# Optimization experiments

Hardware: AMD Instinct MI355X
Metric: run time of the kernel (lower is better)

Reference implementation:

```python
import jax, jax.numpy as jnp
import numpy as np

# DCNv2 config (matches init_kwargs)
STRIDE, PAD, DIL = 1, 1, 1
KH, KW = 3, 3
K = KH * KW


def setup_inputs() -> dict:
    key = jax.random.key(0)
    k1, k2, k3, k4 = jax.random.split(key, 4)
    B, C, H, W = 2, 256, 96, 96
    O = 256
    inp = jax.random.normal(k1, (B, C, H, W), jnp.float32)
    # offset channels interleaved (dy, dx) per kernel tap -> 2*K channels
    offset = jax.random.normal(k2, (B, 2 * K, H, W), jnp.float32)
    # modulation mask in [0,1) (sigmoid is applied outside this module in DCN heads)
    mask = jax.random.uniform(k3, (B, K, H, W), jnp.float32)
    n = C * KH * KW
    stdv = 1.0 / float(np.sqrt(n))
    weight = jax.random.uniform(k4, (O, C, KH, KW), jnp.float32, -stdv, stdv)
    bias = jnp.zeros((O,), jnp.float32)
    return {"input": inp, "offset": offset, "mask": mask, "weight": weight, "bias": bias}


def reference(input, offset, mask, weight, bias):
    B, C, H, W = input.shape
    O = weight.shape[0]
    Ho = (H + 2 * PAD - DIL * (KH - 1) - 1) // STRIDE + 1
    Wo = (W + 2 * PAD - DIL * (KW - 1) - 1) // STRIDE + 1

    # learned per-pixel offsets: channel layout [dy_k0, dx_k0, dy_k1, dx_k1, ...]
    dy = offset[:, 0::2]  # [B,K,Ho,Wo]
    dx = offset[:, 1::2]  # [B,K,Ho,Wo]

    ky = (jnp.arange(K) // KW * DIL).astype(jnp.float32)  # kernel tap row offsets
    kx = (jnp.arange(K) % KW * DIL).astype(jnp.float32)   # kernel tap col offsets
    base_y = (jnp.arange(Ho) * STRIDE - PAD).astype(jnp.float32)
    base_x = (jnp.arange(Wo) * STRIDE - PAD).astype(jnp.float32)

    # sampling positions, [B,K,Ho,Wo]
    y = base_y[None, None, :, None] + ky[None, :, None, None] + dy
    x = base_x[None, None, None, :] + kx[None, :, None, None] + dx

    y0 = jnp.floor(y)
    x0 = jnp.floor(x)
    wy = y - y0  # bilinear fractional weights
    wx = x - x0

    inp_flat = input.reshape(B, C, H * W)

    def gather(yi, xi):
        # zero-padded bilinear corner gather: out-of-bounds -> 0
        ii = yi.astype(jnp.int32)
        jj = xi.astype(jnp.int32)
        valid = ((ii >= 0) & (ii < H) & (jj >= 0) & (jj < W)).astype(input.dtype)
        idx = jnp.clip(ii, 0, H - 1) * W + jnp.clip(jj, 0, W - 1)  # [B,K,Ho,Wo]
        v = jnp.take_along_axis(inp_flat, idx.reshape(B, 1, -1), axis=2)  # [B,C,K*Ho*Wo]
        return v * valid.reshape(B, 1, -1)

    v00 = gather(y0, x0)
    v01 = gather(y0, x0 + 1)
    v10 = gather(y0 + 1, x0)
    v11 = gather(y0 + 1, x0 + 1)

    wyf = wy.reshape(B, 1, -1)
    wxf = wx.reshape(B, 1, -1)
    sampled = (v00 * (1 - wyf) * (1 - wxf) + v01 * (1 - wyf) * wxf
               + v10 * wyf * (1 - wxf) + v11 * wyf * wxf)  # [B,C,K*Ho*Wo]

    mod = sampled * mask.reshape(B, 1, -1)           # modulation per tap/pixel
    mod = mod.reshape(B, C, K, Ho * Wo)
    out = jnp.einsum('bcks,ock->bos', mod, weight.reshape(O, C, K)) + bias[None, :, None]
    return out.reshape(B, O, Ho, Wo)
```

## Files before the change

### kernel.cpp

```cpp
#include <hip/hip_runtime.h>
#include <hip/hip_bf16.h>


#define Hh 96
#define Ww 96
#define Cc 256
#define Oo 256
#define Bb 2
#define Kk 9
#define Ss (Hh * Ww)
#define CKTOT (Cc * Kk)

typedef __bf16 bf16x8 __attribute__((ext_vector_type(8)));
typedef __bf16 bf16x2v __attribute__((ext_vector_type(2)));
typedef float f32x16 __attribute__((ext_vector_type(16)));
typedef float f32x2 __attribute__((ext_vector_type(2)));

__device__ __forceinline__ f32x2 up2(unsigned u) {
  f32x2 r;
  r.x = __uint_as_float(u << 16);
  r.y = __uint_as_float(u & 0xffff0000u);
  return r;
}

__device__ __forceinline__ void barrier_lgkm() {
  asm volatile("" ::: "memory");
  __builtin_amdgcn_s_waitcnt(0xC07F);
  __builtin_amdgcn_s_barrier();
  asm volatile("" ::: "memory");
}

__global__ __launch_bounds__(256) void prep(const float* __restrict__ inp,
                                            const float* __restrict__ wsrc,
                                            __bf16* __restrict__ it,
                                            __bf16* __restrict__ wt) {
  __shared__ float tile[64][65];
  const int bx = blockIdx.x;
  const int tid = threadIdx.x;

  if (bx < 1152) {
    const int hw0 = (bx % 144) * 64;
    const int c0 = ((bx / 144) & 3) * 64;
    const int b = bx / 576;
    const int hw_l = tid & 63, cr = tid >> 6;
    const float* src = inp + ((size_t)(b * Cc + c0) * Ss) + hw0;
#pragma unroll
    for (int r = 0; r < 16; ++r) {
      int c_l = r * 4 + cr;
      tile[c_l][hw_l] = src[(size_t)c_l * Ss + hw_l];
    }
    __syncthreads();
    const int cp = (tid & 31) * 2, hr = tid >> 5;
    __bf16* dst = it + ((size_t)(b * Ss + hw0) * Cc) + c0;
#pragma unroll
    for (int r = 0; r < 8; ++r) {
      int hw_s = r * 8 + hr;
      bf16x2v p;
      p.x = (__bf16)tile[cp][hw_s];
      p.y = (__bf16)tile[cp + 1][hw_s];
      *(bf16x2v*)(dst + (size_t)hw_s * Cc + cp) = p;
    }
  } else {
    int i = (bx - 1152) * 256 + tid;
    int j = i & 7;
    int l = (i >> 3) & 63;
    int osub = (i >> 9) & 7;
    int cc = (i >> 12) & 15;
    int kk = i >> 16;
    int o = osub * 32 + (l & 31);
    int ch = cc * 16 + ((l >> 5) << 3) + j;
    wt[i] = (__bf16)wsrc[(o * Cc + ch) * Kk + kk];
  }
}

__global__ __launch_bounds__(512, 4) void dcn_main(
    const __bf16* __restrict__ it,
    const __bf16* __restrict__ wt,
    const float* __restrict__ offset,
    const float* __restrict__ mask,
    const float* __restrict__ bias,
    float* __restrict__ out)
{
  __shared__ __bf16 colT[2][32 * 256];
  __shared__ int4 pa9[9][32];
  __shared__ float4 pw9[9][32];

  const int tid = threadIdx.x;
  const int tile = (blockIdx.x & 7) * 36 + (blockIdx.x >> 3);
  const int s0 = tile * 32;
  const int b = blockIdx.y;
  const int lane = tid & 63;
  const int wv = tid >> 6;
  const int wq = wv & 3;
  const int chh = wv >> 2;
  const int cbase = chh * 8;
  const int sB = lane & 31;
  const int hi = lane >> 5;
  const int fs = tid >> 4;
  const int fg = tid & 15;

  const __bf16* itb = it + (size_t)b * Ss * Cc;

  if (tid < 9 * 32) {
    int kk = tid >> 5;
    int sl = tid & 31;
    int s = s0 + sl;
    int ho = s / Ww;
    int wo = s - ho * Ww;
    float dy = offset[((size_t)(b * 18 + 2 * kk)) * Ss + s];
    float dx = offset[((size_t)(b * 18 + 2 * kk + 1)) * Ss + s];
    float m = mask[((size_t)(b * 9 + kk)) * Ss + s];
    float y = (float)(ho - 1 + kk / 3) + dy;
    float x = (float)(wo - 1 + kk % 3) + dx;
    float fy = floorf(y), fx = floorf(x);
    int y0 = (int)fy, x0 = (int)fx;
    float wy = y - fy, wx = x - fx;
    int y1 = y0 + 1, x1 = x0 + 1;
    float vy0 = (y0 >= 0 && y0 < Hh) ? 1.f : 0.f;
    float vy1 = (y1 >= 0 && y1 < Hh) ? 1.f : 0.f;
    float vx0 = (x0 >= 0 && x0 < Ww) ? 1.f : 0.f;
    float vx1 = (x1 >= 0 && x1 < Ww) ? 1.f : 0.f;
    int y0c = min(max(y0, 0), Hh - 1), y1c = min(max(y1, 0), Hh - 1);
    int x0c = min(max(x0, 0), Ww - 1), x1c = min(max(x1, 0), Ww - 1);
    pa9[kk][sl] = make_int4((y0c * Ww + x0c) * Cc, (y0c * Ww + x1c) * Cc,
                            (y1c * Ww + x0c) * Cc, (y1c * Ww + x1c) * Cc);
    pw9[kk][sl] = make_float4(m * (1.f - wy) * (1.f - wx) * vy0 * vx0,
                              m * (1.f - wy) * wx * vy0 * vx1,
                              m * wy * (1.f - wx) * vy1 * vx0,
                              m * wy * wx * vy1 * vx1);
  }
  __syncthreads();

  f32x16 acc0, acc1;
#pragma unroll
  for (int j = 0; j < 16; ++j) { acc0[j] = 0.f; acc1[j] = 0.f; }

  auto ldW = [&](int kk, int cc, int which) {
    size_t idx = (size_t)((kk * 16 + cc) * 8 + wq * 2 + which);
    return *(const bf16x8*)(wt + (idx << 9) + (lane << 3));
  };
  auto ldB = [&](int buf, int cc) {
    int g = ((2 * cc + hi) ^ (sB & 7)) << 3;
    return *(const bf16x8*)(&colT[buf][sB * 256 + g]);
  };

  for (int kk = 0; kk < Kk; ++kk) {
    const int buf = kk & 1;
    {
      int4 a = pa9[kk][fs];
      float4 wqv = pw9[kk][fs];
      __bf16* drow = &colT[buf][fs * 256];
#pragma unroll
      for (int it2 = 0; it2 < 2; ++it2) {
        int g = fg + it2 * 16;
        const __bf16* p = itb + g * 8;
        uint4 c00 = *(const uint4*)(p + a.x);
        uint4 c01 = *(const uint4*)(p + a.y);
        uint4 c10 = *(const uint4*)(p + a.z);
        uint4 c11 = *(const uint4*)(p + a.w);
        unsigned u0[4] = {c00.x, c00.y, c00.z, c00.w};
        unsigned u1[4] = {c01.x, c01.y, c01.z, c01.w};
        unsigned u2[4] = {c10.x, c10.y, c10.z, c10.w};
        unsigned u3[4] = {c11.x, c11.y, c11.z, c11.w};
        bf16x8 rv;
#pragma unroll
        for (int w = 0; w < 4; ++w) {
          f32x2 r = up2(u0[w]) * wqv.x + up2(u1[w]) * wqv.y +
                    up2(u2[w]) * wqv.z + up2(u3[w]) * wqv.w;
          rv[2 * w] = (__bf16)r.x;
          rv[2 * w + 1] = (__bf16)r.y;
        }
        *(bf16x8*)(drow + ((g ^ (fs & 7)) << 3)) = rv;
      }
    }
    bf16x8 Wacur = ldW(kk, cbase, 0);
    bf16x8 Wbcur = ldW(kk, cbase, 1);
    barrier_lgkm();

    bf16x8 Bcur = ldB(buf, cbase);
#pragma unroll
    for (int cc = 0; cc < 8; ++cc) {
      bf16x8 Bn, Wan, Wbn;
      if (cc < 7) {
        Bn = ldB(buf, cbase + cc + 1);
        Wan = ldW(kk, cbase + cc + 1, 0);
        Wbn = ldW(kk, cbase + cc + 1, 1);
      }
      acc0 = __builtin_amdgcn_mfma_f32_32x32x16_bf16(Wacur, Bcur, acc0, 0, 0, 0);
      acc1 = __builtin_amdgcn_mfma_f32_32x32x16_bf16(Wbcur, Bcur, acc1, 0, 0, 0);
      if (cc < 7) {
        Bcur = Bn;
        Wacur = Wan;
        Wbcur = Wbn;
      }
    }
  }

  __syncthreads();
  float* red = (float*)colT;
  if (chh == 1) {
#pragma unroll
    for (int os = 0; os < 2; ++os)
#pragma unroll
      for (int r = 0; r < 16; ++r)
        red[(os * 16 + r) * 256 + wq * 64 + lane] = (os ? acc1[r] : acc0[r]);
  }
  __syncthreads();

  if (chh == 0) {
    float* ob = out + (size_t)b * Oo * Ss + s0 + sB;
#pragma unroll
    for (int os = 0; os < 2; ++os) {
#pragma unroll
      for (int r = 0; r < 16; ++r) {
        int o = wq * 64 + os * 32 + (r & 3) + 8 * (r >> 2) + 4 * hi;
        float v = (os ? acc1[r] : acc0[r]) +
                  red[(os * 16 + r) * 256 + wq * 64 + lane] + bias[o];
        ob[(size_t)o * Ss] = v;
      }
    }
  }
}

extern "C" void kernel_launch(void* const* d_in, const int* in_sizes, int n_in,
                              void* d_out, int out_size, void* d_ws, size_t ws_size,
                              hipStream_t stream) {
  (void)in_sizes; (void)n_in; (void)out_size; (void)ws_size;
  const float* inp = (const float*)d_in[0];
  const float* offset = (const float*)d_in[1];
  const float* mask = (const float*)d_in[2];
  const float* weight = (const float*)d_in[3];
  const float* bias = (const float*)d_in[4];
  float* out = (float*)d_out;

  __bf16* it = (__bf16*)d_ws;
  __bf16* wt = (__bf16*)((char*)d_ws + (size_t)Bb * Ss * Cc * 2);

  prep<<<3456, 256, 0, stream>>>(inp, weight, it, wt);
  dcn_main<<<dim3(288, Bb), 512, 0, stream>>>(it, wt, offset, mask, bias, out);
}
```

Baseline: 132.1 us.

## Process both batch images per block to reuse weight fragments across batches

Each block now handles the same 32-pixel tile for both batch items, so every weight fragment loaded from global memory feeds two MFMAs instead of one. The grid shrinks from 288x2 to 288 blocks. The colT double buffer is repurposed to hold one buffer per batch, which requires an extra barrier per tap and removes the old overlap between taps. Accumulator registers double, so launch bounds drop to 3 blocks per CU, and with only 288 blocks the GPU may be underfilled.

```diff
diff --git a/kernel.cpp b/kernel.cpp
--- a/kernel.cpp
+++ b/kernel.cpp
@@ -73,7 +73,7 @@
   }
 }
 
-__global__ __launch_bounds__(512, 4) void dcn_main(
+__global__ __launch_bounds__(512, 3) void dcn_main(
     const __bf16* __restrict__ it,
     const __bf16* __restrict__ wt,
     const float* __restrict__ offset,
@@ -82,13 +82,12 @@
     float* __restrict__ out)
 {
   __shared__ __bf16 colT[2][32 * 256];
-  __shared__ int4 pa9[9][32];
-  __shared__ float4 pw9[9][32];
+  __shared__ int4 pa9[2][9][32];
+  __shared__ float4 pw9[2][9][32];
 
   const int tid = threadIdx.x;
   const int tile = (blockIdx.x & 7) * 36 + (blockIdx.x >> 3);
   const int s0 = tile * 32;
-  const int b = blockIdx.y;
   const int lane = tid & 63;
   const int wv = tid >> 6;
   const int wq = wv & 3;
@@ -99,17 +98,17 @@
   const int fs = tid >> 4;
   const int fg = tid & 15;
 
-  const __bf16* itb = it + (size_t)b * Ss * Cc;
-
-  if (tid < 9 * 32) {
-    int kk = tid >> 5;
-    int sl = tid & 31;
+  for (int idx = tid; idx < 2 * 9 * 32; idx += 512) {
+    int bt = idx >= 288 ? 1 : 0;
+    int rem = idx - bt * 288;
+    int kk = rem >> 5;
+    int sl = rem & 31;
     int s = s0 + sl;
     int ho = s / Ww;
     int wo = s - ho * Ww;
-    float dy = offset[((size_t)(b * 18 + 2 * kk)) * Ss + s];
-    float dx = offset[((size_t)(b * 18 + 2 * kk + 1)) * Ss + s];
-    float m = mask[((size_t)(b * 9 + kk)) * Ss + s];
+    float dy = offset[((size_t)(bt * 18 + 2 * kk)) * Ss + s];
+    float dx = offset[((size_t)(bt * 18 + 2 * kk + 1)) * Ss + s];
+    float m = mask[((size_t)(bt * 9 + kk)) * Ss + s];
     float y = (float)(ho - 1 + kk / 3) + dy;
     float x = (float)(wo - 1 + kk % 3) + dx;
     float fy = floorf(y), fx = floorf(x);
@@ -122,38 +121,41 @@
     float vx1 = (x1 >= 0 && x1 < Ww) ? 1.f : 0.f;
     int y0c = min(max(y0, 0), Hh - 1), y1c = min(max(y1, 0), Hh - 1);
     int x0c = min(max(x0, 0), Ww - 1), x1c = min(max(x1, 0), Ww - 1);
-    pa9[kk][sl] = make_int4((y0c * Ww + x0c) * Cc, (y0c * Ww + x1c) * Cc,
-                            (y1c * Ww + x0c) * Cc, (y1c * Ww + x1c) * Cc);
-    pw9[kk][sl] = make_float4(m * (1.f - wy) * (1.f - wx) * vy0 * vx0,
-                              m * (1.f - wy) * wx * vy0 * vx1,
-                              m * wy * (1.f - wx) * vy1 * vx0,
-                              m * wy * wx * vy1 * vx1);
-  }
-  __syncthreads();
-
-  f32x16 acc0, acc1;
-#pragma unroll
-  for (int j = 0; j < 16; ++j) { acc0[j] = 0.f; acc1[j] = 0.f; }
+    pa9[bt][kk][sl] = make_int4((y0c * Ww + x0c) * Cc, (y0c * Ww + x1c) * Cc,
+                                (y1c * Ww + x0c) * Cc, (y1c * Ww + x1c) * Cc);
+    pw9[bt][kk][sl] = make_float4(m * (1.f - wy) * (1.f - wx) * vy0 * vx0,
+                                  m * (1.f - wy) * wx * vy0 * vx1,
+                                  m * wy * (1.f - wx) * vy1 * vx0,
+                                  m * wy * wx * vy1 * vx1);
+  }
+  __syncthreads();
+
+  f32x16 acc00, acc01, acc10, acc11;
+#pragma unroll
+  for (int j = 0; j < 16; ++j) {
+    acc00[j] = 0.f; acc01[j] = 0.f; acc10[j] = 0.f; acc11[j] = 0.f;
+  }
 
   auto ldW = [&](int kk, int cc, int which) {
     size_t idx = (size_t)((kk * 16 + cc) * 8 + wq * 2 + which);
     return *(const bf16x8*)(wt + (idx << 9) + (lane << 3));
   };
-  auto ldB = [&](int buf, int cc) {
+  auto ldB = [&](int bt, int cc) {
     int g = ((2 * cc + hi) ^ (sB & 7)) << 3;
-    return *(const bf16x8*)(&colT[buf][sB * 256 + g]);
+    return *(const bf16x8*)(&colT[bt][sB * 256 + g]);
   };
 
   for (int kk = 0; kk < Kk; ++kk) {
-    const int buf = kk & 1;
-    {
-      int4 a = pa9[kk][fs];
-      float4 wqv = pw9[kk][fs];
-      __bf16* drow = &colT[buf][fs * 256];
+#pragma unroll
+    for (int bt = 0; bt < 2; ++bt) {
+      int4 a = pa9[bt][kk][fs];
+      float4 wqv = pw9[bt][kk][fs];
+      const __bf16* pb = it + (size_t)bt * Ss * Cc;
+      __bf16* drow = &colT[bt][fs * 256];
 #pragma unroll
       for (int it2 = 0; it2 < 2; ++it2) {
         int g = fg + it2 * 16;
-        const __bf16* p = itb + g * 8;
+        const __bf16* p = pb + g * 8;
         uint4 c00 = *(const uint4*)(p + a.x);
         uint4 c01 = *(const uint4*)(p + a.y);
         uint4 c10 = *(const uint4*)(p + a.z);
@@ -177,45 +179,70 @@
     bf16x8 Wbcur = ldW(kk, cbase, 1);
     barrier_lgkm();
 
-    bf16x8 Bcur = ldB(buf, cbase);
+    bf16x8 B0cur = ldB(0, cbase);
+    bf16x8 B1cur = ldB(1, cbase);
 #pragma unroll
     for (int cc = 0; cc < 8; ++cc) {
-      bf16x8 Bn, Wan, Wbn;
+      bf16x8 Wan, Wbn, B0n, B1n;
       if (cc < 7) {
-        Bn = ldB(buf, cbase + cc + 1);
         Wan = ldW(kk, cbase + cc + 1, 0);
         Wbn = ldW(kk, cbase + cc + 1, 1);
-      }
-      acc0 = __builtin_amdgcn_mfma_f32_32x32x16_bf16(Wacur, Bcur, acc0, 0, 0, 0);
-      acc1 = __builtin_amdgcn_mfma_f32_32x32x16_bf16(Wbcur, Bcur, acc1, 0, 0, 0);
+        B0n = ldB(0, cbase + cc + 1);
+        B1n = ldB(1, cbase + cc + 1);
+      }
+      acc00 = __builtin_amdgcn_mfma_f32_32x32x16_bf16(Wacur, B0cur, acc00, 0, 0, 0);
+      acc01 = __builtin_amdgcn_mfma_f32_32x32x16_bf16(Wacur, B1cur, acc01, 0, 0, 0);
+      acc10 = __builtin_amdgcn_mfma_f32_32x32x16_bf16(Wbcur, B0cur, acc10, 0, 0, 0);
+      acc11 = __builtin_amdgcn_mfma_f32_32x32x16_bf16(Wbcur, B1cur, acc11, 0, 0, 0);
       if (cc < 7) {
-        Bcur = Bn;
-        Wacur = Wan;
-        Wbcur = Wbn;
-      }
-    }
-  }
-
-  __syncthreads();
+        Wacur = Wan; Wbcur = Wbn; B0cur = B0n; B1cur = B1n;
+      }
+    }
+    barrier_lgkm();
+  }
+
   float* red = (float*)colT;
   if (chh == 1) {
 #pragma unroll
-    for (int os = 0; os < 2; ++os)
+    for (int which = 0; which < 2; ++which)
 #pragma unroll
       for (int r = 0; r < 16; ++r)
-        red[(os * 16 + r) * 256 + wq * 64 + lane] = (os ? acc1[r] : acc0[r]);
-  }
-  __syncthreads();
-
+        red[(which * 16 + r) * 256 + wq * 64 + lane] =
+            (which ? acc10[r] : acc00[r]);
+  }
+  __syncthreads();
   if (chh == 0) {
-    float* ob = out + (size_t)b * Oo * Ss + s0 + sB;
-#pragma unroll
-    for (int os = 0; os < 2; ++os) {
+    float* ob = out + s0 + sB;
+#pragma unroll
+    for (int which = 0; which < 2; ++which) {
 #pragma unroll
       for (int r = 0; r < 16; ++r) {
-        int o = wq * 64 + os * 32 + (r & 3) + 8 * (r >> 2) + 4 * hi;
-        float v = (os ? acc1[r] : acc0[r]) +
-                  red[(os * 16 + r) * 256 + wq * 64 + lane] + bias[o];
+        int o = wq * 64 + which * 32 + (r & 3) + 8 * (r >> 2) + 4 * hi;
+        float v = (which ? acc10[r] : acc00[r]) +
+                  red[(which * 16 + r) * 256 + wq * 64 + lane] + bias[o];
+        ob[(size_t)o * Ss] = v;
+      }
+    }
+  }
+  __syncthreads();
+  if (chh == 1) {
+#pragma unroll
+    for (int which = 0; which < 2; ++which)
+#pragma unroll
+      for (int r = 0; r < 16; ++r)
+        red[(which * 16 + r) * 256 + wq * 64 + lane] =
+            (which ? acc11[r] : acc01[r]);
+  }
+  __syncthreads();
+  if (chh == 0) {
+    float* ob = out + (size_t)Oo * Ss + s0 + sB;
+#pragma unroll
+    for (int which = 0; which < 2; ++which) {
+#pragma unroll
+      for (int r = 0; r < 16; ++r) {
+        int o = wq * 64 + which * 32 + (r & 3) + 8 * (r >> 2) + 4 * hi;
+        float v = (which ? acc11[r] : acc01[r]) +
+                  red[(which * 16 + r) * 256 + wq * 64 + lane] + bias[o];
         ob[(size_t)o * Ss] = v;
       }
     }
@@ -237,5 +264,5 @@
   __bf16* wt = (__bf16*)((char*)d_ws + (size_t)Bb * Ss * Cc * 2);
 
   prep<<<3456, 256, 0, stream>>>(inp, weight, it, wt);
-  dcn_main<<<dim3(288, Bb), 512, 0, stream>>>(it, wt, offset, mask, bias, out);
-}
+  dcn_main<<<288, 512, 0, stream>>>(it, wt, offset, mask, bias, out);
+}
```

Measured after the change: 144.4 us. +9.3%, slower.
